# Kernel optimization log

Measured on AMD Instinct MI355X. Metric: run time of the kernel, lower is better.

Reference implementation:

```python
import jax, jax.numpy as jnp
import numpy as np
from jax import lax


def setup_inputs() -> dict:
    key = jax.random.key(0)
    ks = jax.random.split(key, 10)
    B, T, Din, U = 64, 256, 128, 1024
    def rn(k, shape, sc=0.02):
        return jax.random.normal(k, shape, jnp.float32) * sc
    return {
        "inputs": jax.random.normal(ks[0], (B, T, Din), jnp.float32),
        "We1": rn(ks[1], (Din, U)), "be1": jnp.zeros((U,), jnp.float32),
        "We2": rn(ks[2], (U, U)),   "be2": jnp.zeros((U,), jnp.float32),
        "W1": rn(ks[3], (U, U)),    "b1": jnp.zeros((U,), jnp.float32),
        "W2": rn(ks[4], (U, U)),    "b2": jnp.zeros((U,), jnp.float32),
        "V": rn(ks[5], (U, 1)),     "bV": jnp.zeros((1,), jnp.float32),
        "Wk": rn(ks[6], (U, 4 * U)),
        "Wr": rn(ks[7], (U, 4 * U)),
        "bl": jnp.zeros((4 * U,), jnp.float32),
        "Wo": rn(ks[8], (U, 1)),    "bo": jnp.zeros((1,), jnp.float32),
        "seq_len": 256,
    }


def reference(inputs, We1, be1, We2, be2, W1, b1, W2, b2, V, bV,
              Wk, Wr, bl, Wo, bo, seq_len):
    B = inputs.shape[0]
    U = Wr.shape[0]
    f32 = inputs.dtype
    # Frozen embedding ANN, applied per timestep: [B,T,Din] -> [B,T,U]
    h1 = jax.nn.relu(inputs @ We1 + be1)
    x = jax.nn.relu(h1 @ We2 + be2)            # attention values [B,T,U]
    # W2(values) is constant across decode steps; hoist out of the loop.
    keys = x @ W2 + b2                          # [B,T,U]

    def step(carry, _):
        h, c = carry                            # [B,U] each
        # Bahdanau attention: score = V(tanh(W1(q) + W2(values)))
        q = h @ W1 + b1                         # [B,U]
        score = jnp.tanh(q[:, None, :] + keys) @ V + bV   # [B,T,1]
        attw = jax.nn.softmax(score, axis=1)    # softmax over time axis
        ctx = jnp.sum(attw * x, axis=1)         # context vector [B,U]
        # Keras LSTM cell (gate order i,f,g,o; sigmoid recurrent, tanh act)
        z = ctx @ Wk + h @ Wr + bl              # [B,4U]
        i, f, g, o = jnp.split(z, 4, axis=-1)
        i = jax.nn.sigmoid(i)
        f = jax.nn.sigmoid(f)
        g = jnp.tanh(g)
        o = jax.nn.sigmoid(o)
        c_new = f * c + i * g
        h_new = o * jnp.tanh(c_new)
        out = h_new @ Wo + bo                   # [B,1]
        return (h_new, c_new), out

    init = (jnp.zeros((B, U), f32), jnp.zeros((B, U), f32))
    _, outs = lax.scan(step, init, None, length=seq_len)   # [seq_len,B,1]
    return jnp.squeeze(outs, axis=2)            # [seq_len, B]
```

## Files before the change

### kernel.cpp

```cpp
#include <hip/hip_runtime.h>

#define U_ 1024
#define B_ 64
#define T_ 256
#define DIN_ 128
#define BT_ (B_*T_)
#define G_ 1024
#define NWB 576

#define FA_L   0
#define RELA_L 64
#define CE_L   128
#define CZ_L   192
#define CX_L   208
#define RELX_L 272
#define CC_L   336
#define RELC_L 352
#define SYNC_N (416*16)

typedef __attribute__((ext_vector_type(4))) float f32x4;
typedef __attribute__((ext_vector_type(8))) short s16x8;
typedef __attribute__((ext_vector_type(4))) unsigned short u16x4;
typedef unsigned long long u64;

union U64F2 { u64 q; float f[2]; };
union U64H4 { u64 q; unsigned short h[4]; };

__device__ inline unsigned short f2bf(float x){
  unsigned u = __float_as_uint(x);
  u += 0x7FFFu + ((u >> 16) & 1u);
  return (unsigned short)(u >> 16);
}
__device__ inline float bf2f(unsigned short b){ return __uint_as_float(((unsigned)b) << 16); }
__device__ inline float fast_rcp(float x){ return __builtin_amdgcn_rcpf(x); }
__device__ inline float fast_tanh(float x){
  float e = __expf(2.0f * x);
  return 1.0f - 2.0f * fast_rcp(e + 1.0f);
}
__device__ inline float fast_sig(float x){
  return fast_rcp(1.0f + __expf(-x));
}

__device__ inline u64 ald64(const u64* p){
  return __hip_atomic_load((u64*)p, __ATOMIC_RELAXED, __HIP_MEMORY_SCOPE_AGENT);
}
__device__ inline void ast64(u64* p, u64 v){
  __hip_atomic_store(p, v, __ATOMIC_RELAXED, __HIP_MEMORY_SCOPE_AGENT);
}
__device__ inline float aldf(const float* p){
  return __hip_atomic_load((float*)p, __ATOMIC_RELAXED, __HIP_MEMORY_SCOPE_AGENT);
}
__device__ inline void astf(float* p, float v){
  __hip_atomic_store(p, v, __ATOMIC_RELAXED, __HIP_MEMORY_SCOPE_AGENT);
}
__device__ inline unsigned ald32(const unsigned* p){
  return __hip_atomic_load((unsigned*)p, __ATOMIC_RELAXED, __HIP_MEMORY_SCOPE_AGENT);
}
__device__ inline void ast32(unsigned* p, unsigned v){
  __hip_atomic_store(p, v, __ATOMIC_RELAXED, __HIP_MEMORY_SCOPE_AGENT);
}
__device__ inline void aadd32(unsigned* p, unsigned v){
  __hip_atomic_fetch_add(p, v, __ATOMIC_RELAXED, __HIP_MEMORY_SCOPE_AGENT);
}
__device__ inline s16x8 frag_ald(const u64* p){
  u64 a = ald64(p), b = ald64(p + 1);
  union { u64 q[2]; s16x8 v; } x; x.q[0] = a; x.q[1] = b; return x.v;
}

__device__ inline void wait1(unsigned* line, unsigned tgt){
  if (threadIdx.x == 0){
    while (ald32(line) < tgt) __builtin_amdgcn_s_sleep(2);
  }
  __syncthreads();
}

__device__ inline float score8(s16x8 k0, s16x8 k1, const float* tqv, const float* Vv){
  float s = 0.f;
  #pragma unroll
  for (int e = 0; e < 8; ++e){
    float kf = bf2f((unsigned short)k0[e]);
    float num = tqv[e] + kf;
    float den = fmaf(tqv[e], kf, 1.0f);
    s += Vv[e] * num * fast_rcp(den);
  }
  #pragma unroll
  for (int e = 0; e < 8; ++e){
    float kf = bf2f((unsigned short)k1[e]);
    float num = tqv[8+e] + kf;
    float den = fmaf(tqv[8+e], kf, 1.0f);
    s += Vv[8+e] * num * fast_rcp(den);
  }
  return s;
}

__global__ void init_kernel(float* c, unsigned short* hb0, unsigned short* hb1,
                            unsigned* sync, const float* V, float* vbound){
  int i = blockIdx.x * 256 + threadIdx.x;
  if (i < B_*U_){ c[i] = 0.f; hb0[i] = 0; hb1[i] = 0; }
  if (i < SYNC_N) sync[i] = 0u;
  if (blockIdx.x == 0){
    __shared__ float red[4];
    int t = threadIdx.x, lane = t & 63, w = t >> 6;
    float s = fabsf(V[t]) + fabsf(V[t+256]) + fabsf(V[t+512]) + fabsf(V[t+768]);
    #pragma unroll
    for (int mk = 32; mk >= 1; mk >>= 1) s += __shfl_xor(s, mk, 64);
    if (lane == 0) red[w] = s;
    __syncthreads();
    if (t == 0) vbound[0] = red[0] + red[1] + red[2] + red[3];
  }
}

__global__ void transpose_bf_kernel(const float* W, unsigned short* WT, int K, int N){
  int ktiles = K >> 5;
  int kb = blockIdx.x % ktiles, nb = blockIdx.x / ktiles;
  __shared__ float tile[32][33];
  int x = threadIdx.x & 31, y8 = threadIdx.x >> 5;
  #pragma unroll
  for (int i = 0; i < 4; ++i){
    int y = y8*4 + i;
    tile[y][x] = W[(size_t)(kb*32 + y)*N + nb*32 + x];
  }
  __syncthreads();
  #pragma unroll
  for (int i = 0; i < 4; ++i){
    int y = y8*4 + i;
    WT[(size_t)(nb*32 + y)*K + kb*32 + x] = f2bf(tile[x][y]);
  }
}

template<int AF32>
__global__ __launch_bounds__(256) void gemm_embed(const void* Aptr, const unsigned short* BT,
                                                  const float* bias, unsigned short* Cout,
                                                  int K, int act){
  int nb = blockIdx.x & 15, mb = blockIdx.x >> 4;
  int lane = threadIdx.x & 63, w = threadIdx.x >> 6;
  int l15 = lane & 15, quad = lane >> 4;
  int m0 = mb*64 + w*16;
  int arow = m0 + l15;
  f32x4 acc[4];
  #pragma unroll
  for (int nt = 0; nt < 4; ++nt) acc[nt] = (f32x4){0.f,0.f,0.f,0.f};

  for (int k0 = 0; k0 < K; k0 += 32){
    int koff = k0 + quad*8;
    s16x8 a8;
    if (AF32){
      const float* ap = (const float*)Aptr + (size_t)arow*K + koff;
      f32x4 lo = *(const f32x4*)ap;
      f32x4 hi = *(const f32x4*)(ap + 4);
      a8[0]=(short)f2bf(lo[0]); a8[1]=(short)f2bf(lo[1]); a8[2]=(short)f2bf(lo[2]); a8[3]=(short)f2bf(lo[3]);
      a8[4]=(short)f2bf(hi[0]); a8[5]=(short)f2bf(hi[1]); a8[6]=(short)f2bf(hi[2]); a8[7]=(short)f2bf(hi[3]);
    } else {
      a8 = *(const s16x8*)((const unsigned short*)Aptr + (size_t)arow*K + koff);
    }
    #pragma unroll
    for (int nt = 0; nt < 4; ++nt){
      const unsigned short* bp = BT + (size_t)(nb*64 + nt*16 + l15)*K + koff;
      s16x8 b8 = *(const s16x8*)bp;
      acc[nt] = __builtin_amdgcn_mfma_f32_16x16x32_bf16(a8, b8, acc[nt], 0, 0, 0);
    }
  }
  #pragma unroll
  for (int nt = 0; nt < 4; ++nt){
    int col = nb*64 + nt*16 + l15;
    float bv = bias[col];
    #pragma unroll
    for (int r = 0; r < 4; ++r){
      int row = m0 + quad*4 + r;
      float v = acc[nt][r] + bv;
      v = (act == 0) ? fmaxf(v, 0.f) : fast_tanh(v);
      Cout[(size_t)row*U_ + col] = f2bf(v);
    }
  }
}

struct SeqP {
  const unsigned short *W1Tb, *WkTb, *WrTb, *tk, *xv;
  const float *b1, *bl, *V, *Wo, *bo, *vbound;
  float *tq, *ew, *c, *zh, *out_part, *out;
  unsigned short *ctxb, *hb0, *hb1;
  unsigned *sync;
};

__device__ inline void out_reduce(const SeqP& p, int b, int sidx, float* smem,
                                  int t, int lane, int w){
  float v = aldf(&p.out_part[b*256 + t]);
  #pragma unroll
  for (int mk = 32; mk >= 1; mk >>= 1) v += __shfl_xor(v, mk, 64);
  if (lane == 0) smem[w] = v;
  __syncthreads();
  if (t == 0) p.out[sidx*64 + b] = smem[0] + smem[1] + smem[2] + smem[3] + p.bo[0];
  __syncthreads();
}

__global__ __launch_bounds__(256, 4) void seq_kernel(SeqP p){
  const int bi = blockIdx.x;
  const int t  = threadIdx.x;
  const int lane = t & 63, w = t >> 6;
  const int l15 = lane & 15, quad = lane >> 4;
  __shared__ __align__(16) unsigned short lfrag[16384];
  __shared__ __align__(16) float smem[1664];
  unsigned* sync = p.sync;
  const float Mb = p.vbound[0];

  if (bi < NWB){
    const unsigned short* wsrc;
    if (bi < 64)       wsrc = p.W1Tb + (size_t)(bi*16 + l15)*U_;
    else if (bi < 320) wsrc = p.WrTb + (size_t)((bi - 64)*16 + l15)*U_;
    else               wsrc = p.WkTb + (size_t)((l15 >> 2)*U_ + (bi - 320)*4 + (l15 & 3))*U_;
    for (int it = w; it < 32; it += 4)
      *(s16x8*)&lfrag[it*512 + lane*8] = *(const s16x8*)(wsrc + it*32 + quad*8);
  } else {
    const unsigned short* ksrc = p.tk + (size_t)((bi >> 4)*T_ + (bi & 15)*16)*U_;
    for (int r = w; r < 16; r += 4){
      *(s16x8*)&lfrag[r*1024 +       lane*8] = *(const s16x8*)(ksrc + (size_t)r*U_ + lane*16);
      *(s16x8*)&lfrag[r*1024 + 512 + lane*8] = *(const s16x8*)(ksrc + (size_t)r*U_ + lane*16 + 8);
    }
  }
  __syncthreads();

  u64* tqu  = (u64*)p.tq;
  u64* ewu  = (u64*)p.ew;
  u64* zhu  = (u64*)p.zh;
  u64* ctxu = (u64*)p.ctxb;

  for (int step = 0; step < T_; ++step){
    const u64* hbRu = (const u64*)((step & 1) ? p.hb1 : p.hb0);
    u64*       hbWu = (u64*)((step & 1) ? p.hb0 : p.hb1);

    if (bi < 64){
      wait1(&sync[(RELC_L + (bi & 63))*16], (unsigned)step);
      int jcol = bi*16 + l15;
      int rbase = (w*16 + l15) << 8;
      f32x4 acc = (f32x4){0.f,0.f,0.f,0.f};
      #pragma unroll 8
      for (int k = 0; k < U_; k += 32){
        s16x8 a8 = frag_ald(hbRu + rbase + ((k + quad*8) >> 2));
        s16x8 b8 = *(const s16x8*)&lfrag[(k >> 5)*512 + lane*8];
        acc = __builtin_amdgcn_mfma_f32_16x16x32_bf16(a8, b8, acc, 0, 0, 0);
      }
      float bj = p.b1[jcol];
      float* tqs = smem;
      #pragma unroll
      for (int r = 0; r < 4; ++r)
        tqs[l15*68 + w*16 + quad*4 + r] = fast_tanh(acc[r] + bj);
      __syncthreads();
      if (t < 64){
        int ub64 = (t*U_ + bi*16) >> 1;
        #pragma unroll
        for (int cc = 0; cc < 16; cc += 2){
          U64F2 x;
          x.f[0] = tqs[(cc+0)*68 + t];
          x.f[1] = tqs[(cc+1)*68 + t];
          ast64(tqu + ub64 + (cc >> 1), x.q);
        }
      }
      __syncthreads();
      if (t == 0) ast32(&sync[(FA_L + bi)*16], (unsigned)(step + 1));
      if (bi == 0){
        if (t < 64){
          unsigned tgt = (unsigned)(step + 1);
          for (;;){
            bool ok = ald32(&sync[(FA_L + t)*16]) >= tgt;
            if (__ballot(ok) == ~0ull) break;
            __builtin_amdgcn_s_sleep(1);
          }
          ast32(&sync[(RELA_L + t)*16], tgt);
        }
      }
    } else if (bi < 320){
      wait1(&sync[(RELC_L + (bi & 63))*16], (unsigned)step);
      int bz = bi - 64;
      int rbase = (w*16 + l15) << 8;
      int jc0 = bz*16 + l15;
      f32x4 acc0 = (f32x4){0.f,0.f,0.f,0.f};
      #pragma unroll 8
      for (int k = 0; k < U_; k += 32){
        s16x8 a8 = frag_ald(hbRu + rbase + ((k + quad*8) >> 2));
        s16x8 b8 = *(const s16x8*)&lfrag[(k >> 5)*512 + lane*8];
        acc0 = __builtin_amdgcn_mfma_f32_16x16x32_bf16(a8, b8, acc0, 0, 0, 0);
      }
      float bl0 = p.bl[jc0];
      int brow = w*16 + quad*4;
      U64F2 x;
      int i0 = (jc0*64 + brow) >> 1;
      x.f[0] = acc0[0] + bl0; x.f[1] = acc0[1] + bl0; ast64(zhu + i0, x.q);
      x.f[0] = acc0[2] + bl0; x.f[1] = acc0[3] + bl0; ast64(zhu + i0 + 1, x.q);
      __syncthreads();
      if (t == 0) aadd32(&sync[(CZ_L + ((bi - 64) & 15))*16], 1u);
    } else if (bi >= 960){
      if (bi == 960){
        if (step > 0){
          if (t < 64){
            unsigned tgt = 16u * (unsigned)step;
            for (;;){
              bool ok = (t < 16) ? (ald32(&sync[(CC_L + t)*16]) >= tgt) : true;
              if (__ballot(ok) == ~0ull) break;
              __builtin_amdgcn_s_sleep(1);
            }
            ast32(&sync[(RELC_L + t)*16], (unsigned)step);
          }
          __syncthreads();
          out_reduce(p, 0, step - 1, smem, t, lane, w);
        }
      } else {
        wait1(&sync[(RELC_L + (bi & 63))*16], (unsigned)step);
        if (step > 0) out_reduce(p, bi - 960, step - 1, smem, t, lane, w);
      }
    }

    wait1(&sync[(RELA_L + (bi & 63))*16], (unsigned)(step + 1));
    {
      int b = bi >> 4, tg = bi & 15;
      float tqv[16], Vv[16];
      int tqb = (b*U_ + lane*16) >> 1;
      #pragma unroll
      for (int i = 0; i < 8; ++i){
        U64F2 x; x.q = ald64(tqu + tqb + i);
        tqv[2*i] = x.f[0]; tqv[2*i+1] = x.f[1];
      }
      const float* Vp = p.V + lane*16;
      #pragma unroll
      for (int i = 0; i < 16; i += 4) *(f32x4*)&Vv[i] = *(const f32x4*)(Vp + i);
      int trow = tg*16 + w*4;
      float sr[4];
      if (bi >= NWB){
        #pragma unroll
        for (int rr = 0; rr < 4; ++rr){
          int rl = w*4 + rr;
          s16x8 k0 = *(const s16x8*)&lfrag[rl*1024 +       lane*8];
          s16x8 k1 = *(const s16x8*)&lfrag[rl*1024 + 512 + lane*8];
          sr[rr] = score8(k0, k1, tqv, Vv);
        }
      } else {
        const unsigned short* kp = p.tk + (size_t)(b*T_ + trow)*U_ + lane*16;
        #pragma unroll
        for (int rr = 0; rr < 4; ++rr){
          s16x8 k0 = *(const s16x8*)(kp + (size_t)rr*U_);
          s16x8 k1 = *(const s16x8*)(kp + (size_t)rr*U_ + 8);
          sr[rr] = score8(k0, k1, tqv, Vv);
        }
      }
      #pragma unroll
      for (int mk = 32; mk >= 1; mk >>= 1){
        #pragma unroll
        for (int rr = 0; rr < 4; ++rr) sr[rr] += __shfl_xor(sr[rr], mk, 64);
      }
      if (lane == 0){
        int eb = (b*T_ + trow) >> 1;
        #pragma unroll
        for (int j = 0; j < 2; ++j){
          U64F2 x;
          x.f[0] = __expf(sr[2*j]   - Mb);
          x.f[1] = __expf(sr[2*j+1] - Mb);
          ast64(ewu + eb + j, x.q);
        }
      }
    }
    __syncthreads();
    if (t == 0) aadd32(&sync[(CE_L + (bi >> 4))*16], 1u);

    wait1(&sync[(CE_L + (bi >> 4))*16], 16u * (unsigned)(step + 1));
    {
      int b = bi >> 4, ug = bi & 15;
      float* ewL = smem;
      float* tmp = smem + 256;
      float* red = smem + 272;
      if (t < 128){
        U64F2 x; x.q = ald64(ewu + b*128 + t);
        ewL[2*t] = x.f[0]; ewL[2*t+1] = x.f[1];
      }
      __syncthreads();
      float e = ewL[t];
      float sum = e;
      #pragma unroll
      for (int mk = 32; mk >= 1; mk >>= 1) sum += __shfl_xor(sum, mk, 64);
      if (lane == 0) tmp[w] = sum;
      __syncthreads();
      float rd = fast_rcp(tmp[0] + tmp[1] + tmp[2] + tmp[3]);

      int ui = t & 15, tgp = t >> 4;
      int u = ug*64 + ui*4;
      const unsigned short* xp = p.xv + (size_t)b*T_*U_ + u;
      f32x4 a = (f32x4){0.f,0.f,0.f,0.f};
      #pragma unroll 4
      for (int t8 = tgp; t8 < T_; t8 += 16){
        float wg = ewL[t8];
        u16x4 x4 = *(const u16x4*)(xp + (size_t)t8*U_);
        a[0] = fmaf(wg, bf2f(x4[0]), a[0]);
        a[1] = fmaf(wg, bf2f(x4[1]), a[1]);
        a[2] = fmaf(wg, bf2f(x4[2]), a[2]);
        a[3] = fmaf(wg, bf2f(x4[3]), a[3]);
      }
      *(f32x4*)&red[(tgp*16 + ui)*4] = a;
      __syncthreads();
      if (t < 16){
        f32x4 r = (f32x4){0.f,0.f,0.f,0.f};
        #pragma unroll
        for (int g = 0; g < 16; ++g){
          f32x4 rr = *(f32x4*)&red[(g*16 + t)*4];
          r[0]+=rr[0]; r[1]+=rr[1]; r[2]+=rr[2]; r[3]+=rr[3];
        }
        U64H4 cv;
        cv.h[0]=f2bf(r[0]*rd); cv.h[1]=f2bf(r[1]*rd); cv.h[2]=f2bf(r[2]*rd); cv.h[3]=f2bf(r[3]*rd);
        ast64(ctxu + b*256 + ug*16 + t, cv.q);
      }
    }
    __syncthreads();
    if (t == 0) aadd32(&sync[(CX_L + (bi & 63))*16], 1u);

    if (bi == 576){
      unsigned tgt = 16u * (unsigned)(step + 1);
      if (w == 0){
        for (;;){
          bool ok = ald32(&sync[(CX_L + lane)*16]) >= tgt;
          if (__ballot(ok) == ~0ull) break;
          __builtin_amdgcn_s_sleep(1);
        }
      } else if (w == 1){
        for (;;){
          bool ok = (lane < 16) ? (ald32(&sync[(CZ_L + lane)*16]) >= tgt) : true;
          if (__ballot(ok) == ~0ull) break;
          __builtin_amdgcn_s_sleep(1);
        }
      }
      __syncthreads();
      if (t < 64) ast32(&sync[(RELX_L + t)*16], (unsigned)(step + 1));
    }

    if (bi >= 320 && bi < NWB){
      wait1(&sync[(RELX_L + (bi & 63))*16], (unsigned)(step + 1));
      int cb = bi - 320;
      int ub = cb*4;
      int gate = l15 >> 2, uo = l15 & 3;
      int jcol = gate*U_ + ub + uo;
      int rbase = (w*16 + l15) << 8;
      f32x4 acc = (f32x4){0.f,0.f,0.f,0.f};
      #pragma unroll 8
      for (int k = 0; k < U_; k += 32){
        s16x8 a8 = frag_ald(ctxu + rbase + ((k + quad*8) >> 2));
        s16x8 b8 = *(const s16x8*)&lfrag[(k >> 5)*512 + lane*8];
        acc = __builtin_amdgcn_mfma_f32_16x16x32_bf16(a8, b8, acc, 0, 0, 0);
      }
      int brow = w*16 + quad*4;
      int zi0 = (jcol*64 + brow) >> 1;
      U64F2 z0, z1;
      z0.q = ald64(zhu + zi0); z1.q = ald64(zhu + zi0 + 1);
      acc[0] += z0.f[0]; acc[1] += z0.f[1]; acc[2] += z1.f[0]; acc[3] += z1.f[1];
      float* zs = smem;
      float* hs = smem + 1088;
      float* op = smem + 1344;
      *(f32x4*)&zs[l15*68 + brow] = acc;
      __syncthreads();
      {
        int b = t & 63, ui = t >> 6;
        int u = ub + ui;
        float zi = zs[(0*4 + ui)*68 + b];
        float zf = zs[(1*4 + ui)*68 + b];
        float zg = zs[(2*4 + ui)*68 + b];
        float zo = zs[(3*4 + ui)*68 + b];
        float ig = fast_sig(zi), fg = fast_sig(zf);
        float gg = fast_tanh(zg), og = fast_sig(zo);
        float cold = p.c[u*64 + b];
        float cn = fg*cold + ig*gg;
        float hn = og * fast_tanh(cn);
        p.c[u*64 + b] = cn;
        hs[ui*64 + b] = hn;
        op[ui*64 + b] = hn * p.Wo[u];
      }
      __syncthreads();
      if (t < 64){
        U64H4 h0;
        #pragma unroll
        for (int k = 0; k < 4; ++k) h0.h[k] = f2bf(hs[k*64 + t]);
        ast64(hbWu + t*256 + cb, h0.q);
        float po = op[t] + op[64 + t] + op[128 + t] + op[192 + t];
        astf(&p.out_part[t*256 + cb], po);
      }
      __syncthreads();
      if (t == 0) aadd32(&sync[(CC_L + ((bi - 320) & 15))*16], 1u);
    }
  }

  if (bi == 960){
    if (t < 64){
      unsigned tgt = 16u * (unsigned)T_;
      for (;;){
        bool ok = (t < 16) ? (ald32(&sync[(CC_L + t)*16]) >= tgt) : true;
        if (__ballot(ok) == ~0ull) break;
        __builtin_amdgcn_s_sleep(1);
      }
      ast32(&sync[(RELC_L + t)*16], (unsigned)T_);
    }
    __syncthreads();
    out_reduce(p, 0, T_ - 1, smem, t, lane, w);
  } else if (bi > 960){
    wait1(&sync[(RELC_L + (bi & 63))*16], (unsigned)T_);
    out_reduce(p, bi - 960, T_ - 1, smem, t, lane, w);
  }
}

extern "C" void kernel_launch(void* const* d_in, const int* in_sizes, int n_in,
                              void* d_out, int out_size, void* d_ws, size_t ws_size,
                              hipStream_t stream){
  const float* inputs = (const float*)d_in[0];
  const float* We1 = (const float*)d_in[1];
  const float* be1 = (const float*)d_in[2];
  const float* We2 = (const float*)d_in[3];
  const float* be2 = (const float*)d_in[4];
  const float* W1  = (const float*)d_in[5];
  const float* b1  = (const float*)d_in[6];
  const float* W2  = (const float*)d_in[7];
  const float* b2  = (const float*)d_in[8];
  const float* V   = (const float*)d_in[9];
  const float* Wk  = (const float*)d_in[11];
  const float* Wr  = (const float*)d_in[12];
  const float* bl  = (const float*)d_in[13];
  const float* Wo  = (const float*)d_in[14];
  const float* bo  = (const float*)d_in[15];
  float* out = (float*)d_out;

  char* ws = (char*)d_ws;
  size_t off = 0;
  auto alloc = [&](size_t bytes) -> void* {
    void* pp = ws + off;
    off = (off + bytes + 255) & ~(size_t)255;
    return pp;
  };
  unsigned short* We1Tb = (unsigned short*)alloc((size_t)1024*128*2);
  unsigned short* We2Tb = (unsigned short*)alloc((size_t)1024*1024*2);
  unsigned short* W2Tb  = (unsigned short*)alloc((size_t)1024*1024*2);
  unsigned short* W1Tb  = (unsigned short*)alloc((size_t)1024*1024*2);
  unsigned short* WkTb  = (unsigned short*)alloc((size_t)4096*1024*2);
  unsigned short* WrTb  = (unsigned short*)alloc((size_t)4096*1024*2);
  unsigned short* h1tk  = (unsigned short*)alloc((size_t)BT_*U_*2);
  unsigned short* xv    = (unsigned short*)alloc((size_t)BT_*U_*2);
  float*          c     = (float*)alloc((size_t)B_*U_*4);
  unsigned short* hb0   = (unsigned short*)alloc((size_t)B_*U_*2);
  unsigned short* hb1   = (unsigned short*)alloc((size_t)B_*U_*2);
  unsigned short* ctxb  = (unsigned short*)alloc((size_t)B_*U_*2);
  float*          tq    = (float*)alloc((size_t)B_*U_*4);
  float*          ew    = (float*)alloc((size_t)B_*T_*4);
  float*          zh    = (float*)alloc((size_t)4*U_*64*4);
  float*          out_part = (float*)alloc((size_t)64*256*4);
  unsigned*       sync  = (unsigned*)alloc((size_t)SYNC_N*4);
  float*          vbound= (float*)alloc(256);
  if (ws_size < off) return;

  init_kernel<<<256, 256, 0, stream>>>(c, hb0, hb1, sync, V, vbound);
  transpose_bf_kernel<<<(128/32)*(1024/32),  256, 0, stream>>>(We1, We1Tb, 128, 1024);
  transpose_bf_kernel<<<(1024/32)*(1024/32), 256, 0, stream>>>(We2, We2Tb, 1024, 1024);
  transpose_bf_kernel<<<(1024/32)*(1024/32), 256, 0, stream>>>(W2,  W2Tb,  1024, 1024);
  transpose_bf_kernel<<<(1024/32)*(1024/32), 256, 0, stream>>>(W1,  W1Tb,  1024, 1024);
  transpose_bf_kernel<<<(1024/32)*(4096/32), 256, 0, stream>>>(Wk,  WkTb,  1024, 4096);
  transpose_bf_kernel<<<(1024/32)*(4096/32), 256, 0, stream>>>(Wr,  WrTb,  1024, 4096);

  gemm_embed<1><<<4096, 256, 0, stream>>>((const void*)inputs, We1Tb, be1, h1tk, DIN_, 0);
  gemm_embed<0><<<4096, 256, 0, stream>>>((const void*)h1tk,   We2Tb, be2, xv,   U_,   0);
  gemm_embed<0><<<4096, 256, 0, stream>>>((const void*)xv,     W2Tb,  b2,  h1tk, U_,   1);

  SeqP sp;
  sp.W1Tb = W1Tb; sp.WkTb = WkTb; sp.WrTb = WrTb; sp.tk = h1tk; sp.xv = xv;
  sp.b1 = b1; sp.bl = bl; sp.V = V; sp.Wo = Wo; sp.bo = bo; sp.vbound = vbound;
  sp.tq = tq; sp.ew = ew; sp.c = c; sp.zh = zh;
  sp.out_part = out_part; sp.out = out;
  sp.ctxb = ctxb; sp.hb0 = hb0; sp.hb1 = hb1; sp.sync = sync;
  seq_kernel<<<dim3(G_), dim3(256), 0, stream>>>(sp);
}
```

Baseline: 12.61 ms.

## Consolidate recurrent and context GEMM work into fewer blocks with 4 tiles each

```diff
diff --git a/kernel.cpp b/kernel.cpp
--- a/kernel.cpp
+++ b/kernel.cpp
@@ -6,7 +6,7 @@
 #define DIN_ 128
 #define BT_ (B_*T_)
 #define G_ 1024
-#define NWB 576
+#define NWB 192
 
 #define FA_L   0
 #define RELA_L 64
@@ -182,14 +182,13 @@
   unsigned *sync;
 };
 
-__device__ inline void out_reduce(const SeqP& p, int b, int sidx, float* smem,
-                                  int t, int lane, int w){
-  float v = aldf(&p.out_part[b*256 + t]);
-  #pragma unroll
-  for (int mk = 32; mk >= 1; mk >>= 1) v += __shfl_xor(v, mk, 64);
-  if (lane == 0) smem[w] = v;
-  __syncthreads();
-  if (t == 0) p.out[sidx*64 + b] = smem[0] + smem[1] + smem[2] + smem[3] + p.bo[0];
+__device__ inline void out_reduce(const SeqP& p, int b, int sidx, int t, int lane, int w){
+  if (w == 0){
+    float v = aldf(&p.out_part[b*64 + lane]);
+    #pragma unroll
+    for (int mk = 32; mk >= 1; mk >>= 1) v += __shfl_xor(v, mk, 64);
+    if (lane == 0) p.out[sidx*64 + b] = v + p.bo[0];
+  }
   __syncthreads();
 }
 
@@ -206,8 +205,8 @@
   if (bi < NWB){
     const unsigned short* wsrc;
     if (bi < 64)       wsrc = p.W1Tb + (size_t)(bi*16 + l15)*U_;
-    else if (bi < 320) wsrc = p.WrTb + (size_t)((bi - 64)*16 + l15)*U_;
-    else               wsrc = p.WkTb + (size_t)((l15 >> 2)*U_ + (bi - 320)*4 + (l15 & 3))*U_;
+    else if (bi < 128) wsrc = p.WrTb + (size_t)((bi - 64)*64 + l15)*U_;
+    else               wsrc = p.WkTb + (size_t)((l15 >> 2)*U_ + (bi - 128)*16 + (l15 & 3))*U_;
     for (int it = w; it < 32; it += 4)
       *(s16x8*)&lfrag[it*512 + lane*8] = *(const s16x8*)(wsrc + it*32 + quad*8);
   } else {
@@ -268,31 +267,42 @@
           ast32(&sync[(RELA_L + t)*16], tgt);
         }
       }
-    } else if (bi < 320){
+    } else if (bi < 128){
       wait1(&sync[(RELC_L + (bi & 63))*16], (unsigned)step);
-      int bz = bi - 64;
+      int zb = bi - 64;
       int rbase = (w*16 + l15) << 8;
-      int jc0 = bz*16 + l15;
-      f32x4 acc0 = (f32x4){0.f,0.f,0.f,0.f};
-      #pragma unroll 8
+      int jc0 = zb*64 + l15;
+      const unsigned short* bp1 = p.WrTb + (size_t)(jc0 + 16)*U_;
+      const unsigned short* bp2 = p.WrTb + (size_t)(jc0 + 32)*U_;
+      const unsigned short* bp3 = p.WrTb + (size_t)(jc0 + 48)*U_;
+      f32x4 ac0 = (f32x4){0.f,0.f,0.f,0.f}, ac1 = ac0, ac2 = ac0, ac3 = ac0;
+      #pragma unroll 4
       for (int k = 0; k < U_; k += 32){
-        s16x8 a8 = frag_ald(hbRu + rbase + ((k + quad*8) >> 2));
-        s16x8 b8 = *(const s16x8*)&lfrag[(k >> 5)*512 + lane*8];
-        acc0 = __builtin_amdgcn_mfma_f32_16x16x32_bf16(a8, b8, acc0, 0, 0, 0);
-      }
-      float bl0 = p.bl[jc0];
+        int ko = k + quad*8;
+        s16x8 a8 = frag_ald(hbRu + rbase + (ko >> 2));
+        ac0 = __builtin_amdgcn_mfma_f32_16x16x32_bf16(a8, *(const s16x8*)&lfrag[(k>>5)*512 + lane*8], ac0, 0, 0, 0);
+        ac1 = __builtin_amdgcn_mfma_f32_16x16x32_bf16(a8, *(const s16x8*)(bp1 + ko), ac1, 0, 0, 0);
+        ac2 = __builtin_amdgcn_mfma_f32_16x16x32_bf16(a8, *(const s16x8*)(bp2 + ko), ac2, 0, 0, 0);
+        ac3 = __builtin_amdgcn_mfma_f32_16x16x32_bf16(a8, *(const s16x8*)(bp3 + ko), ac3, 0, 0, 0);
+      }
       int brow = w*16 + quad*4;
-      U64F2 x;
-      int i0 = (jc0*64 + brow) >> 1;
-      x.f[0] = acc0[0] + bl0; x.f[1] = acc0[1] + bl0; ast64(zhu + i0, x.q);
-      x.f[0] = acc0[2] + bl0; x.f[1] = acc0[3] + bl0; ast64(zhu + i0 + 1, x.q);
+      #pragma unroll
+      for (int nt = 0; nt < 4; ++nt){
+        f32x4 acc = (nt==0) ? ac0 : (nt==1) ? ac1 : (nt==2) ? ac2 : ac3;
+        int jc = jc0 + nt*16;
+        float bl0 = p.bl[jc];
+        U64F2 x;
+        int i0 = (jc*64 + brow) >> 1;
+        x.f[0] = acc[0] + bl0; x.f[1] = acc[1] + bl0; ast64(zhu + i0, x.q);
+        x.f[0] = acc[2] + bl0; x.f[1] = acc[3] + bl0; ast64(zhu + i0 + 1, x.q);
+      }
       __syncthreads();
       if (t == 0) aadd32(&sync[(CZ_L + ((bi - 64) & 15))*16], 1u);
     } else if (bi >= 960){
       if (bi == 960){
         if (step > 0){
           if (t < 64){
-            unsigned tgt = 16u * (unsigned)step;
+            unsigned tgt = 4u * (unsigned)step;
             for (;;){
               bool ok = (t < 16) ? (ald32(&sync[(CC_L + t)*16]) >= tgt) : true;
               if (__ballot(ok) == ~0ull) break;
@@ -301,27 +311,37 @@
             ast32(&sync[(RELC_L + t)*16], (unsigned)step);
           }
           __syncthreads();
-          out_reduce(p, 0, step - 1, smem, t, lane, w);
+          out_reduce(p, 0, step - 1, t, lane, w);
         }
       } else {
         wait1(&sync[(RELC_L + (bi & 63))*16], (unsigned)step);
-        if (step > 0) out_reduce(p, bi - 960, step - 1, smem, t, lane, w);
+        if (step > 0) out_reduce(p, bi - 960, step - 1, t, lane, w);
       }
     }
 
     wait1(&sync[(RELA_L + (bi & 63))*16], (unsigned)(step + 1));
     {
       int b = bi >> 4, tg = bi & 15;
-      float tqv[16], Vv[16];
-      int tqb = (b*U_ + lane*16) >> 1;
-      #pragma unroll
-      for (int i = 0; i < 8; ++i){
-        U64F2 x; x.q = ald64(tqu + tqb + i);
-        tqv[2*i] = x.f[0]; tqv[2*i+1] = x.f[1];
-      }
+      float* tqS = smem + 272;
+      {
+        U64F2 x0, x1;
+        x0.q = ald64(tqu + b*512 + t*2);
+        x1.q = ald64(tqu + b*512 + t*2 + 1);
+        int r0 = t >> 2, i0 = (t*4) & 15;
+        tqS[r0*17 + i0    ] = x0.f[0];
+        tqS[r0*17 + i0 + 1] = x0.f[1];
+        tqS[r0*17 + i0 + 2] = x1.f[0];
+        tqS[r0*17 + i0 + 3] = x1.f[1];
+      }
+      float Vv[16];
       const float* Vp = p.V + lane*16;
       #pragma unroll
       for (int i = 0; i < 16; i += 4) *(f32x4*)&Vv[i] = *(const f32x4*)(Vp + i);
+      __syncthreads();
+      float tqv[16];
+      #pragma unroll
+      for (int i = 0; i < 16; ++i) tqv[i] = tqS[lane*17 + i];
+
       int trow = tg*16 + w*4;
       float sr[4];
       if (bi >= NWB){
@@ -336,8 +356,8 @@
         const unsigned short* kp = p.tk + (size_t)(b*T_ + trow)*U_ + lane*16;
         #pragma unroll
         for (int rr = 0; rr < 4; ++rr){
-          s16x8 k0 = *(const s16x8*)(kp + (size_t)rr*U_);
-          s16x8 k1 = *(const s16x8*)(kp + (size_t)rr*U_ + 8);
+          s16x8 k0 = __builtin_nontemporal_load((const s16x8*)(kp + (size_t)rr*U_));
+          s16x8 k1 = __builtin_nontemporal_load((const s16x8*)(kp + (size_t)rr*U_ + 8));
           sr[rr] = score8(k0, k1, tqv, Vv);
         }
       }
@@ -383,7 +403,7 @@
       int u = ug*64 + ui*4;
       const unsigned short* xp = p.xv + (size_t)b*T_*U_ + u;
       f32x4 a = (f32x4){0.f,0.f,0.f,0.f};
-      #pragma unroll 4
+      #pragma unroll 8
       for (int t8 = tgp; t8 < T_; t8 += 16){
         float wg = ewL[t8];
         u16x4 x4 = *(const u16x4*)(xp + (size_t)t8*U_);
@@ -410,16 +430,17 @@
     if (t == 0) aadd32(&sync[(CX_L + (bi & 63))*16], 1u);
 
     if (bi == 576){
-      unsigned tgt = 16u * (unsigned)(step + 1);
+      unsigned tgtx = 16u * (unsigned)(step + 1);
+      unsigned tgtz = 4u  * (unsigned)(step + 1);
       if (w == 0){
         for (;;){
-          bool ok = ald32(&sync[(CX_L + lane)*16]) >= tgt;
+          bool ok = ald32(&sync[(CX_L + lane)*16]) >= tgtx;
           if (__ballot(ok) == ~0ull) break;
           __builtin_amdgcn_s_sleep(1);
         }
       } else if (w == 1){
         for (;;){
-          bool ok = (lane < 16) ? (ald32(&sync[(CZ_L + lane)*16]) >= tgt) : true;
+          bool ok = (lane < 16) ? (ald32(&sync[(CZ_L + lane)*16]) >= tgtz) : true;
           if (__ballot(ok) == ~0ull) break;
           __builtin_amdgcn_s_sleep(1);
         }
@@ -428,63 +449,84 @@
       if (t < 64) ast32(&sync[(RELX_L + t)*16], (unsigned)(step + 1));
     }
 
-    if (bi >= 320 && bi < NWB){
+    if (bi >= 128 && bi < NWB){
       wait1(&sync[(RELX_L + (bi & 63))*16], (unsigned)(step + 1));
-      int cb = bi - 320;
-      int ub = cb*4;
+      int cb = bi - 128;
+      int ub = cb*16;
       int gate = l15 >> 2, uo = l15 & 3;
-      int jcol = gate*U_ + ub + uo;
       int rbase = (w*16 + l15) << 8;
-      f32x4 acc = (f32x4){0.f,0.f,0.f,0.f};
-      #pragma unroll 8
+      const unsigned short* bq1 = p.WkTb + (size_t)(gate*U_ + ub + 4  + uo)*U_;
+      const unsigned short* bq2 = p.WkTb + (size_t)(gate*U_ + ub + 8  + uo)*U_;
+      const unsigned short* bq3 = p.WkTb + (size_t)(gate*U_ + ub + 12 + uo)*U_;
+      f32x4 ac0 = (f32x4){0.f,0.f,0.f,0.f}, ac1 = ac0, ac2 = ac0, ac3 = ac0;
+      #pragma unroll 4
       for (int k = 0; k < U_; k += 32){
-        s16x8 a8 = frag_ald(ctxu + rbase + ((k + quad*8) >> 2));
-        s16x8 b8 = *(const s16x8*)&lfrag[(k >> 5)*512 + lane*8];
-        acc = __builtin_amdgcn_mfma_f32_16x16x32_bf16(a8, b8, acc, 0, 0, 0);
+        int ko = k + quad*8;
+        s16x8 a8 = frag_ald(ctxu + rbase + (ko >> 2));
+        ac0 = __builtin_amdgcn_mfma_f32_16x16x32_bf16(a8, *(const s16x8*)&lfrag[(k>>5)*512 + lane*8], ac0, 0, 0, 0);
+        ac1 = __builtin_amdgcn_mfma_f32_16x16x32_bf16(a8, *(const s16x8*)(bq1 + ko), ac1, 0, 0, 0);
+        ac2 = __builtin_amdgcn_mfma_f32_16x16x32_bf16(a8, *(const s16x8*)(bq2 + ko), ac2, 0, 0, 0);
+        ac3 = __builtin_amdgcn_mfma_f32_16x16x32_bf16(a8, *(const s16x8*)(bq3 + ko), ac3, 0, 0, 0);
       }
       int brow = w*16 + quad*4;
-      int zi0 = (jcol*64 + brow) >> 1;
-      U64F2 z0, z1;
-      z0.q = ald64(zhu + zi0); z1.q = ald64(zhu + zi0 + 1);
-      acc[0] += z0.f[0]; acc[1] += z0.f[1]; acc[2] += z1.f[0]; acc[3] += z1.f[1];
+      U64F2 zpre[8];
+      #pragma unroll
+      for (int nt = 0; nt < 4; ++nt){
+        int jcol = gate*U_ + ub + nt*4 + uo;
+        int zi0 = (jcol*64 + brow) >> 1;
+        zpre[2*nt].q   = ald64(zhu + zi0);
+        zpre[2*nt+1].q = ald64(zhu + zi0 + 1);
+      }
       float* zs = smem;
       float* hs = smem + 1088;
       float* op = smem + 1344;
-      *(f32x4*)&zs[l15*68 + brow] = acc;
-      __syncthreads();
-      {
-        int b = t & 63, ui = t >> 6;
-        int u = ub + ui;
-        float zi = zs[(0*4 + ui)*68 + b];
-        float zf = zs[(1*4 + ui)*68 + b];
-        float zg = zs[(2*4 + ui)*68 + b];
-        float zo = zs[(3*4 + ui)*68 + b];
-        float ig = fast_sig(zi), fg = fast_sig(zf);
-        float gg = fast_tanh(zg), og = fast_sig(zo);
-        float cold = p.c[u*64 + b];
-        float cn = fg*cold + ig*gg;
-        float hn = og * fast_tanh(cn);
-        p.c[u*64 + b] = cn;
-        hs[ui*64 + b] = hn;
-        op[ui*64 + b] = hn * p.Wo[u];
-      }
+      int eb = t & 63, ui = t >> 6;
+      float popart = 0.f;
+      #pragma unroll
+      for (int nt = 0; nt < 4; ++nt){
+        f32x4 acc = (nt==0) ? ac0 : (nt==1) ? ac1 : (nt==2) ? ac2 : ac3;
+        acc[0] += zpre[2*nt].f[0];   acc[1] += zpre[2*nt].f[1];
+        acc[2] += zpre[2*nt+1].f[0]; acc[3] += zpre[2*nt+1].f[1];
+        *(f32x4*)&zs[l15*68 + brow] = acc;
+        __syncthreads();
+        {
+          int u = ub + nt*4 + ui;
+          float zi_ = zs[(0*4 + ui)*68 + eb];
+          float zf_ = zs[(1*4 + ui)*68 + eb];
+          float zg_ = zs[(2*4 + ui)*68 + eb];
+          float zo_ = zs[(3*4 + ui)*68 + eb];
+          float ig = fast_sig(zi_), fg = fast_sig(zf_);
+          float gg = fast_tanh(zg_), og = fast_sig(zo_);
+          float cold = p.c[u*64 + eb];
+          float cn = fg*cold + ig*gg;
+          float hn = og * fast_tanh(cn);
+          p.c[u*64 + eb] = cn;
+          hs[ui*64 + eb] = hn;
+          popart = fmaf(hn, p.Wo[u], popart);
+        }
+        __syncthreads();
+        if (t < 64){
+          U64H4 h0;
+          #pragma unroll
+          for (int kk = 0; kk < 4; ++kk) h0.h[kk] = f2bf(hs[kk*64 + t]);
+          ast64(hbWu + t*256 + cb*4 + nt, h0.q);
+        }
+        __syncthreads();
+      }
+      op[ui*64 + eb] = popart;
       __syncthreads();
       if (t < 64){
-        U64H4 h0;
-        #pragma unroll
-        for (int k = 0; k < 4; ++k) h0.h[k] = f2bf(hs[k*64 + t]);
-        ast64(hbWu + t*256 + cb, h0.q);
         float po = op[t] + op[64 + t] + op[128 + t] + op[192 + t];
-        astf(&p.out_part[t*256 + cb], po);
-      }
-      __syncthreads();
-      if (t == 0) aadd32(&sync[(CC_L + ((bi - 320) & 15))*16], 1u);
+        astf(&p.out_part[t*64 + cb], po);
+      }
+      __syncthreads();
+      if (t == 0) aadd32(&sync[(CC_L + (cb & 15))*16], 1u);
     }
   }
 
   if (bi == 960){
     if (t < 64){
-      unsigned tgt = 16u * (unsigned)T_;
+      unsigned tgt = 4u * (unsigned)T_;
       for (;;){
         bool ok = (t < 16) ? (ald32(&sync[(CC_L + t)*16]) >= tgt) : true;
         if (__ballot(ok) == ~0ull) break;
@@ -493,10 +535,10 @@
       ast32(&sync[(RELC_L + t)*16], (unsigned)T_);
     }
     __syncthreads();
-    out_reduce(p, 0, T_ - 1, smem, t, lane, w);
+    out_reduce(p, 0, T_ - 1, t, lane, w);
   } else if (bi > 960){
     wait1(&sync[(RELC_L + (bi & 63))*16], (unsigned)T_);
-    out_reduce(p, bi - 960, T_ - 1, smem, t, lane, w);
+    out_reduce(p, bi - 960, T_ - 1, t, lane, w);
   }
 }
 
@@ -542,7 +584,7 @@
   float*          tq    = (float*)alloc((size_t)B_*U_*4);
   float*          ew    = (float*)alloc((size_t)B_*T_*4);
   float*          zh    = (float*)alloc((size_t)4*U_*64*4);
-  float*          out_part = (float*)alloc((size_t)64*256*4);
+  float*          out_part = (float*)alloc((size_t)64*64*4);
   unsigned*       sync  = (unsigned*)alloc((size_t)SYNC_N*4);
   float*          vbound= (float*)alloc(256);
   if (ws_size < off) return;
```

Measured after the change: 22.77 ms. 1.81x slower.
